# Performance work log

Measured on AMD Instinct MI355X. Metric: run time of the kernel, lower is better.

Reference implementation:

```python
import jax, jax.numpy as jnp
import numpy as np

E = 512        # embed_dim == AutoNCP output_size (motor neurons)
UNITS = 1024   # ncp_units (inter + command + motor)
B = 64         # batch
T = 1024       # sequence length
LN_EPS = 1e-5
SPARSITY = 0.5  # AutoNCP default sparsity_level


def _ncp_sizes():
    rem = UNITS - E
    n_cmd = max(int(0.4 * rem), 1)
    n_inter = rem - n_cmd
    return n_inter, n_cmd, E


def _fanout_mask(rng, n_src, n_dst, fanout):
    # each source neuron connects to `fanout` random targets (NCP-style wiring)
    m = np.zeros((n_src, n_dst), np.float32)
    idx = np.argsort(rng.random((n_src, n_dst)), axis=1)[:, :fanout]
    m[np.arange(n_src)[:, None], idx] = 1.0
    return m


def setup_inputs() -> dict:
    key = jax.random.key(0)
    rng = np.random.default_rng(22222)
    n_inter, n_cmd, n_motor = _ncp_sizes()
    density = 1.0 - SPARSITY
    sensory_fanout = max(int(n_inter * density), 1)
    inter_fanout = max(int(n_cmd * density), 1)
    motor_fanin = max(int(n_cmd * density), 1)
    m0 = _fanout_mask(rng, E, n_inter, sensory_fanout)        # sensory -> inter
    m1 = _fanout_mask(rng, n_inter, n_cmd, inter_fanout)      # inter -> command
    m2 = _fanout_mask(rng, n_motor, n_cmd, motor_fanin).T     # command -> motor (fanin per motor)

    def full_mask(m_in, h):
        # WiredCfCCell: concat ones for the recurrent (hidden) part, then transpose
        # -> mask shape [h, in + h], matching Linear weight [h, in + h]
        return jnp.asarray(np.concatenate([m_in, np.ones((h, h), np.float32)], axis=0).T)

    masks = [full_mask(m0, n_inter), full_mask(m1, n_cmd), full_mask(m2, n_motor)]
    ins = [E, n_inter, n_cmd]
    hs = [n_inter, n_cmd, n_motor]
    d = {}
    ks = jax.random.split(key, 32)
    ki = 0
    for l in range(3):
        fan_in = ins[l] + hs[l]
        scale = float(1.0 / np.sqrt(fan_in))
        for nm in ["ff1", "ff2", "ta", "tb"]:
            d[f"w_{nm}_{l}"] = jax.random.uniform(ks[ki], (hs[l], fan_in), jnp.float32, -scale, scale)
            ki += 1
            d[f"b_{nm}_{l}"] = jnp.zeros((hs[l],), jnp.float32)
        d[f"mask_{l}"] = masks[l]
    d["x"] = jax.random.normal(ks[ki], (B, T, E), jnp.float32)
    d["h0"] = jnp.zeros((B, UNITS), jnp.float32)
    d["ln_gamma"] = jnp.ones((E,), jnp.float32)
    d["ln_beta"] = jnp.zeros((E,), jnp.float32)
    return d


def _cell(z, w1, b1, w2, b2, wa, ba, wb, bb, m):
    # CfCCell (default mode, no backbone), ts = 1.0; sparsity mask on ff1/ff2 only
    ff1 = jnp.tanh(z @ (w1 * m).T + b1)
    ff2 = jnp.tanh(z @ (w2 * m).T + b2)
    t = jax.nn.sigmoid(z @ wa.T + ba + (z @ wb.T + bb))  # sigmoid(t_a * 1.0 + t_b)
    return ff1 * (1.0 - t) + t * ff2


def reference(x, h0, ln_gamma, ln_beta,
              w_ff1_0, b_ff1_0, w_ff2_0, b_ff2_0, w_ta_0, b_ta_0, w_tb_0, b_tb_0, mask_0,
              w_ff1_1, b_ff1_1, w_ff2_1, b_ff2_1, w_ta_1, b_ta_1, w_tb_1, b_tb_1, mask_1,
              w_ff1_2, b_ff1_2, w_ff2_2, b_ff2_2, w_ta_2, b_ta_2, w_tb_2, b_tb_2, mask_2):
    n_inter, n_cmd, _ = _ncp_sizes()
    # LayerNorm over embed_dim
    mu = jnp.mean(x, axis=-1, keepdims=True)
    var = jnp.mean(jnp.square(x - mu), axis=-1, keepdims=True)
    xn = (x - mu) * jax.lax.rsqrt(var + LN_EPS) * ln_gamma + ln_beta
    p0 = (w_ff1_0, b_ff1_0, w_ff2_0, b_ff2_0, w_ta_0, b_ta_0, w_tb_0, b_tb_0, mask_0)
    p1 = (w_ff1_1, b_ff1_1, w_ff2_1, b_ff2_1, w_ta_1, b_ta_1, w_tb_1, b_tb_1, mask_1)
    p2 = (w_ff1_2, b_ff1_2, w_ff2_2, b_ff2_2, w_ta_2, b_ta_2, w_tb_2, b_tb_2, mask_2)

    def step(h, xt):
        h_i, h_c, h_m = jnp.split(h, [n_inter, n_inter + n_cmd], axis=1)
        hi = _cell(jnp.concatenate([xt, h_i], axis=1), *p0)   # inter layer
        hc = _cell(jnp.concatenate([hi, h_c], axis=1), *p1)   # command layer
        hm = _cell(jnp.concatenate([hc, h_m], axis=1), *p2)   # motor layer (block output)
        return jnp.concatenate([hi, hc, hm], axis=1), hm

    h_final, ys = jax.lax.scan(step, h0, jnp.swapaxes(xn, 0, 1))
    y = jnp.swapaxes(ys, 0, 1)  # [B, T, E]; dropout is identity in eval mode
    return y, h_final
```

## Files before the change

### kernel.cpp

```cpp
#include <hip/hip_runtime.h>

typedef __attribute__((ext_vector_type(8))) short short8;
typedef __attribute__((ext_vector_type(4))) float f32x4;
typedef unsigned short ushort_t;
typedef unsigned long long u64_t;

#define T_STEPS 1024
#define NWG 132
#define NWG_MT 33


#define PACK0 0
#define PACK1 1064960
#define PACK2 1517568

#define HI_P (64*320)
#define HC_P (64*224)
#define HM_P (64*512)

#define WS_BAR   0
#define WS_MU    16384
#define WS_RSTD  278528
#define WS_HI    540672
#define WS_HC    704512
#define WS_HM    819200
#define WS_PACK  1081344

__device__ __forceinline__ ushort_t f2bf(float f) {
  union { float f; unsigned u; } un; un.f = f;
  unsigned r = (un.u + 0x7fffu + ((un.u >> 16) & 1u)) >> 16;
  return (ushort_t)r;
}

__device__ __forceinline__ void st2(ushort_t* p, ushort_t v) {
  __hip_atomic_store(p, v, __ATOMIC_RELAXED, __HIP_MEMORY_SCOPE_SYSTEM);
}
__device__ __forceinline__ u64_t ld8(const ushort_t* p) {
  return __hip_atomic_load((const u64_t*)p, __ATOMIC_RELAXED, __HIP_MEMORY_SCOPE_SYSTEM);
}
__device__ __forceinline__ unsigned ldf(const unsigned* p) {
  return __hip_atomic_load(p, __ATOMIC_RELAXED, __HIP_MEMORY_SCOPE_SYSTEM);
}
__device__ __forceinline__ void stf(unsigned* p, unsigned v) {
  __hip_atomic_store(p, v, __ATOMIC_RELAXED, __HIP_MEMORY_SCOPE_SYSTEM);
}

__global__ __launch_bounds__(256) void ln_stats(const float* __restrict__ x,
                                                float* __restrict__ mu,
                                                float* __restrict__ rstd) {
  const int row = blockIdx.x * 4 + (threadIdx.x >> 6);
  const int lane = threadIdx.x & 63;
  const float* xr = x + (size_t)row * 512;
  float4 v0 = *(const float4*)(xr + lane * 8);
  float4 v1 = *(const float4*)(xr + lane * 8 + 4);
  float s = v0.x + v0.y + v0.z + v0.w + v1.x + v1.y + v1.z + v1.w;
  float q = v0.x*v0.x + v0.y*v0.y + v0.z*v0.z + v0.w*v0.w
          + v1.x*v1.x + v1.y*v1.y + v1.z*v1.z + v1.w*v1.w;
  for (int m = 1; m <= 32; m <<= 1) {
    s += __shfl_xor(s, m, 64);
    q += __shfl_xor(q, m, 64);
  }
  if (lane == 0) {
    float mean = s * (1.f / 512.f);
    float var = q * (1.f / 512.f) - mean * mean;
    mu[row] = mean;
    rstd[row] = rsqrtf(var + 1e-5f);
  }
}

__global__ void init_h(const float* __restrict__ h0,
                       ushort_t* hi, ushort_t* hc, ushort_t* hm) {
  int i = blockIdx.x * 256 + threadIdx.x;
  if (i >= 64 * 1056) return;
  int b = i / 1056, c = i % 1056;
  if (c < 320) {
    ushort_t v = (c < 308) ? f2bf(h0[b * 1024 + c]) : 0;
#pragma unroll
    for (int p = 0; p < 4; ++p) st2(hi + p * HI_P + b * 320 + c, v);
  } else if (c < 544) {
    int col = c - 320;
    ushort_t v = (col < 204) ? f2bf(h0[b * 1024 + 308 + col]) : 0;
#pragma unroll
    for (int p = 0; p < 4; ++p) st2(hc + p * HC_P + b * 224 + col, v);
  } else {
    int col = c - 544;
    ushort_t v = f2bf(h0[b * 1024 + 512 + col]);
#pragma unroll
    for (int p = 0; p < 4; ++p) st2(hm + p * HM_P + b * 512 + col, v);
  }
}

struct PackP {
  const float* w[12];
  const float* msk[3];
  ushort_t* pack;
};

__global__ __launch_bounds__(256) void ncp_pack(PackP P) {
  int u = blockIdx.x * 256 + threadIdx.x;
  int layer, rem, KB, K, H, s0p, s0l, s1l;
  size_t base;
  if (u < 133120)      { layer = 0; rem = u;          KB = 26; K = 820; H = 308; s0p = 512; s0l = 512; s1l = 308; base = PACK0; }
  else if (u < 189696) { layer = 1; rem = u - 133120; KB = 17; K = 512; H = 204; s0p = 320; s0l = 308; s1l = 204; base = PACK1; }
  else if (u < 378112) { layer = 2; rem = u - 189696; KB = 23; K = 716; H = 512; s0p = 224; s0l = 204; s1l = 512; base = PACK2; }
  else return;
  const int lane = rem & 63;
  const int mat = (rem >> 6) & 3;
  const int kb = (rem >> 8) % KB;
  const int nt = (rem >> 8) / KB;
  const float* W = P.w[layer * 4 + mat];
  const float* M = (mat < 2) ? P.msk[layer] : nullptr;
  const int n = nt * 16 + (lane & 15);
  const int kbase = kb * 32 + ((lane >> 4) << 3);
  ushort_t* dst = P.pack + base + (size_t)rem * 8;
#pragma unroll
  for (int j = 0; j < 8; ++j) {
    const int kp = kbase + j;
    int ko;
    if (kp < s0p) ko = (kp < s0l) ? kp : -1;
    else { const int ks = kp - s0p; ko = (ks < s1l) ? (s0l + ks) : -1; }
    float v = 0.f;
    if (n < H && ko >= 0) {
      v = W[(size_t)n * K + ko];
      if (M) v *= M[(size_t)n * K + ko];
    }
    dst[j] = f2bf(v);
  }
}

struct MainP {
  const float* x;
  const float* gamma;
  const float* beta;
  const float* bias[12];
  const float* mu;
  const float* rstd;
  ushort_t* hi;
  ushort_t* hc;
  ushort_t* hm;
  const ushort_t* pack;
  unsigned* bar;
  float* y;
  float* hfin;
};

#define MAXKB 13

template<int KBT>
__device__ __forceinline__ void load_w(const ushort_t* __restrict__ bp, int lane,
                                       short8 (*w)[4]) {
#pragma unroll
  for (int kb = 0; kb < KBT; ++kb) {
    const ushort_t* q = bp + (size_t)kb * 2048 + lane * 8;
    w[kb][0] = *(const short8*)(q);
    w[kb][1] = *(const short8*)(q + 512);
    w[kb][2] = *(const short8*)(q + 1024);
    w[kb][3] = *(const short8*)(q + 1536);
  }
}

template<int KBT>
__device__ __forceinline__ void span_reg(const short8 (*w)[4],
                                         const ushort_t* __restrict__ lds, int lane,
                                         f32x4& a0, f32x4& a1, f32x4& a2, f32x4& a3) {
#pragma unroll
  for (int kb = 0; kb < KBT; ++kb) {
    short8 av = *(const short8*)(lds + (size_t)(kb * 64 + lane) * 8);
    a0 = __builtin_amdgcn_mfma_f32_16x16x32_bf16(av, w[kb][0], a0, 0, 0, 0);
    a1 = __builtin_amdgcn_mfma_f32_16x16x32_bf16(av, w[kb][1], a1, 0, 0, 0);
    a2 = __builtin_amdgcn_mfma_f32_16x16x32_bf16(av, w[kb][2], a2, 0, 0, 0);
    a3 = __builtin_amdgcn_mfma_f32_16x16x32_bf16(av, w[kb][3], a3, 0, 0, 0);
  }
}

template<int H, int STP>
__device__ __forceinline__ void epi_h(const f32x4* A, int nt, int lane, int mtile,
                                      const float* __restrict__ bp1, const float* __restrict__ bp2,
                                      const float* __restrict__ bpa, const float* __restrict__ bpb,
                                      ushort_t* __restrict__ hout, float* vk) {
  const int n = nt * 16 + (lane & 15);
  const int r0 = (lane >> 4) << 2;
#pragma unroll
  for (int j = 0; j < 4; ++j) vk[j] = 0.f;
  if (n < H) {
    float c1 = bp1[n], c2 = bp2[n], ca = bpa[n], cb = bpb[n];
#pragma unroll
    for (int j = 0; j < 4; ++j) {
      int brow = mtile * 16 + r0 + j;
      float sg = 1.f / (1.f + __expf(-(A[2][j] + ca + A[3][j] + cb)));
      float f1 = 1.f - 2.f / (1.f + __expf(2.f * (A[0][j] + c1)));
      float f2 = 1.f - 2.f / (1.f + __expf(2.f * (A[1][j] + c2)));
      float v = f1 * (1.f - sg) + sg * f2;
      vk[j] = v;
      st2(hout + (size_t)brow * STP + n, f2bf(v));
    }
  }
}

template<int S1, int ST1, int S2, int ST2>
__device__ __forceinline__ void stage2(ushort_t* __restrict__ r1, const ushort_t* __restrict__ h1,
                                       ushort_t* __restrict__ r2, const ushort_t* __restrict__ h2,
                                       int tid) {
  constexpr int U1 = S1 * 2, U2 = S2 * 2;
  constexpr int I1 = (U1 + 255) / 256;
  constexpr int I2 = (U2 + 255) / 256;
  u64_t a[I1];
  u64_t b[I2 > 0 ? I2 : 1];
#pragma unroll
  for (int i = 0; i < I1; ++i) {
    const int u = tid + i * 256;
    if ((U1 & 255) == 0 || u < U1) {
      const int slot = u >> 1;
      a[i] = ld8(h1 + (slot & 15) * ST1 + (slot >> 6) * 32 + ((slot >> 4) & 3) * 8 + (u & 1) * 4);
    }
  }
  if constexpr (S2 > 0) {
#pragma unroll
    for (int i = 0; i < I2; ++i) {
      const int u = tid + i * 256;
      if ((U2 & 255) == 0 || u < U2) {
        const int slot = u >> 1;
        b[i] = ld8(h2 + (slot & 15) * ST2 + (slot >> 6) * 32 + ((slot >> 4) & 3) * 8 + (u & 1) * 4);
      }
    }
  }
#pragma unroll
  for (int i = 0; i < I1; ++i) {
    const int u = tid + i * 256;
    if ((U1 & 255) == 0 || u < U1) *(u64_t*)(r1 + (size_t)u * 4) = a[i];
  }
  if constexpr (S2 > 0) {
#pragma unroll
    for (int i = 0; i < I2; ++i) {
      const int u = tid + i * 256;
      if ((U2 & 255) == 0 || u < U2) *(u64_t*)(r2 + (size_t)u * 4) = b[i];
    }
  }
}

__device__ __forceinline__ void stage_xn(ushort_t* __restrict__ XN, const MainP& P,
                                         int mtile, int tid, int t) {
#pragma unroll
  for (int i = 0; i < 4; ++i) {
    const int s = tid + i * 256;
    const int ln = s & 63;
    const int brow = mtile * 16 + (ln & 15);
    const int kbase = (s >> 6) * 32 + ((ln >> 4) << 3);
    const float muv = P.mu[brow * T_STEPS + t];
    const float rsv = P.rstd[brow * T_STEPS + t];
    const f32x4* xr = (const f32x4*)(P.x + ((size_t)brow * T_STEPS + t) * 512 + kbase);
    f32x4 xv0 = __builtin_nontemporal_load(xr);
    f32x4 xv1 = __builtin_nontemporal_load(xr + 1);
    const f32x4 g0 = *(const f32x4*)(P.gamma + kbase);
    const f32x4 g1 = *(const f32x4*)(P.gamma + kbase + 4);
    const f32x4 b0 = *(const f32x4*)(P.beta + kbase);
    const f32x4 b1 = *(const f32x4*)(P.beta + kbase + 4);
    short8 w;
#pragma unroll
    for (int j = 0; j < 4; ++j) w[j] = f2bf((xv0[j] - muv) * rsv * g0[j] + b0[j]);
#pragma unroll
    for (int j = 0; j < 4; ++j) w[4 + j] = f2bf((xv1[j] - muv) * rsv * g1[j] + b1[j]);
    *(short8*)(XN + (size_t)s * 8) = w;
  }
}

__device__ __forceinline__ void poll2(const unsigned* wfbase, int lane,
                                      int a1, int c1, unsigned need1,
                                      int a2, int c2, unsigned need2) {
  const unsigned* p = wfbase;
  unsigned need = 0;
  bool act = false;
  if (lane < c1)           { p = wfbase + (a1 + lane) * 16;        need = need1; act = true; }
  else if (lane < c1 + c2) { p = wfbase + (a2 + lane - c1) * 16;   need = need2; act = true; }
  for (;;) {
    unsigned v = act ? ldf(p) : 0xFFFFFFFFu;
    if (__all((int)(v >= need))) break;
    __builtin_amdgcn_s_sleep(1);
  }
}

__global__ __launch_bounds__(256, 1) void ncp_main(MainP P) {
  const int tid = threadIdx.x;
  const int lane = tid & 63;
  const int wv = tid >> 6;
  const int role = wv & 1;
  const int tslot = wv >> 1;
  const int wg = blockIdx.x;
  const int mt = wg / NWG_MT;
  const int r  = wg % NWG_MT;

  __shared__ __align__(16) ushort_t Alds[2688 * 8];
  __shared__ __align__(16) f32x4 pacc[2][256];

  unsigned* wf = P.bar + mt * 1024;
  int a1, c1, a2, c2;
  if (r < 10)      { a1 = 0;  c1 = 10; a2 = 10; c2 = 7;  }
  else if (r < 17) { a1 = 0;  c1 = 17; a2 = 17; c2 = 16; }
  else             { a1 = 10; c1 = 23; a2 = 0;  c2 = 0;  }

  int nt = 0;
  bool valid = true;
  if (r < 10)      nt = r * 2 + tslot;
  else if (r < 17) { nt = (r - 10) * 2 + tslot; valid = (nt < 13); }
  else             nt = (r - 17) * 2 + tslot;

  short8 wreg[MAXKB][4];
  if (valid) {
    if (r < 10) {
      const ushort_t* bp = P.pack + PACK0 + (size_t)nt * 26 * 2048 + (role ? 13 : 0) * 2048;
      load_w<13>(bp, lane, wreg);
    } else if (r < 17) {
      const ushort_t* bp = P.pack + PACK1 + (size_t)nt * 17 * 2048;
      if (role == 0) load_w<9>(bp, lane, wreg);
      else           load_w<8>(bp + 9 * 2048, lane, wreg);
    } else {
      const ushort_t* bp = P.pack + PACK2 + (size_t)nt * 23 * 2048;
      if (role == 0) load_w<12>(bp, lane, wreg);
      else           load_w<11>(bp + 12 * 2048, lane, wreg);
    }
  }

  if (r < 10) stage_xn(Alds, P, mt, tid, 0);

  for (int s = 0; s < T_STEPS + 2; ++s) {
    if (wv == 0) {
      const unsigned needA = (unsigned)s;
      const unsigned needB = (s >= 2) ? (unsigned)(s - 2) : 0u;
      poll2(wf, lane, a1, c1, needA, a2, c2, needB);
    }
    __syncthreads();

    int tstep = 0;
    bool on = false;
    if (r < 10)      { tstep = s;     on = (s < T_STEPS); }
    else if (r < 17) { tstep = s - 1; on = (s >= 1 && s <= T_STEPS) && valid; }
    else             { tstep = s - 2; on = (s >= 2); }
    const bool last = (tstep == T_STEPS - 1);

    if (r < 10) {
      if (s < T_STEPS)
        stage2<640, 320, 0, 0>(Alds + 2048 * 8,
                               P.hi + (((s - 1) & 3) * 64 + mt * 16) * 320,
                               nullptr, nullptr, tid);
    } else if (r < 17) {
      if (s >= 1 && s <= T_STEPS)
        stage2<640, 320, 448, 224>(Alds, P.hi + (((s - 1) & 3) * 64 + mt * 16) * 320,
                                   Alds + 640 * 8,
                                   P.hc + (((s - 2) & 3) * 64 + mt * 16) * 224, tid);
    } else {
      if (s >= 2)
        stage2<448, 224, 1024, 512>(Alds, P.hc + (((s - 2) & 3) * 64 + mt * 16) * 224,
                                    Alds + 448 * 8,
                                    P.hm + (((s - 3) & 3) * 64 + mt * 16) * 512, tid);
    }
    __syncthreads();

    f32x4 A[4];
#pragma unroll
    for (int j = 0; j < 4; ++j) A[j] = {0.f, 0.f, 0.f, 0.f};
    if (on) {
      if (r < 10) {
        const ushort_t* XNc = Alds + (s & 1) * (1024 * 8);
        const ushort_t* HIl = Alds + 2048 * 8;
        if (role == 0) span_reg<13>(wreg, XNc, lane, A[0], A[1], A[2], A[3]);
        else { span_reg<3>(wreg, XNc + 13 * 512, lane, A[0], A[1], A[2], A[3]);
               span_reg<10>(wreg + 3, HIl, lane, A[0], A[1], A[2], A[3]); }
      } else if (r < 17) {
        const ushort_t* HIr = Alds;
        const ushort_t* HCr = Alds + 640 * 8;
        if (role == 0) span_reg<9>(wreg, HIr, lane, A[0], A[1], A[2], A[3]);
        else { span_reg<1>(wreg, HIr + 9 * 512, lane, A[0], A[1], A[2], A[3]);
               span_reg<7>(wreg + 1, HCr, lane, A[0], A[1], A[2], A[3]); }
      } else {
        const ushort_t* HCr = Alds;
        const ushort_t* HMr = Alds + 448 * 8;
        if (role == 0) { span_reg<7>(wreg, HCr, lane, A[0], A[1], A[2], A[3]);
                         span_reg<5>(wreg + 7, HMr, lane, A[0], A[1], A[2], A[3]); }
        else           span_reg<11>(wreg, HMr + 5 * 512, lane, A[0], A[1], A[2], A[3]);
      }
      if (role == 1) {
#pragma unroll
        for (int j = 0; j < 4; ++j) pacc[tslot][j * 64 + lane] = A[j];
      }
    }
    __syncthreads();

    float vk[4];
    if (on && role == 0) {
#pragma unroll
      for (int j = 0; j < 4; ++j) {
        f32x4 p = pacc[tslot][j * 64 + lane];
        A[j][0] += p[0]; A[j][1] += p[1]; A[j][2] += p[2]; A[j][3] += p[3];
      }
      if (r < 10)
        epi_h<308, 320>(A, nt, lane, mt, P.bias[0], P.bias[1], P.bias[2], P.bias[3],
                        P.hi + (tstep & 3) * HI_P, vk);
      else if (r < 17)
        epi_h<204, 224>(A, nt, lane, mt, P.bias[4], P.bias[5], P.bias[6], P.bias[7],
                        P.hc + (tstep & 3) * HC_P, vk);
      else
        epi_h<512, 512>(A, nt, lane, mt, P.bias[8], P.bias[9], P.bias[10], P.bias[11],
                        P.hm + (tstep & 3) * HM_P, vk);
    }
    asm volatile("s_waitcnt vmcnt(0)" ::: "memory");
    __syncthreads();
    if (tid == 0) stf(wf + r * 16, (unsigned)(s + 1));

    if (on && role == 0) {
      const int n_ = nt * 16 + (lane & 15);
      const int r0 = (lane >> 4) << 2;
      const int H_ = (r < 10) ? 308 : ((r < 17) ? 204 : 512);
      const int hoff = (r < 10) ? 0 : ((r < 17) ? 308 : 512);
      if (n_ < H_) {
#pragma unroll
        for (int j = 0; j < 4; ++j) {
          const int brow = mt * 16 + r0 + j;
          if (r >= 17)
            __builtin_nontemporal_store(vk[j], &P.y[((size_t)brow * T_STEPS + tstep) * 512 + n_]);
          if (last)
            __builtin_nontemporal_store(vk[j], &P.hfin[brow * 1024 + hoff + n_]);
        }
      }
    }

    if (r < 10 && s + 1 < T_STEPS)
      stage_xn(Alds + ((s + 1) & 1) * (1024 * 8), P, mt, tid, s + 1);
  }
}

extern "C" void kernel_launch(void* const* d_in, const int* in_sizes, int n_in,
                              void* d_out, int out_size, void* d_ws, size_t ws_size,
                              hipStream_t stream) {
  const float* x     = (const float*)d_in[27];
  const float* h0    = (const float*)d_in[28];
  const float* gamma = (const float*)d_in[29];
  const float* beta  = (const float*)d_in[30];

  char* ws = (char*)d_ws;
  unsigned* bar = (unsigned*)(ws + WS_BAR);
  float* mu   = (float*)(ws + WS_MU);
  float* rstd = (float*)(ws + WS_RSTD);
  ushort_t* hi = (ushort_t*)(ws + WS_HI);
  ushort_t* hc = (ushort_t*)(ws + WS_HC);
  ushort_t* hm = (ushort_t*)(ws + WS_HM);
  ushort_t* pack = (ushort_t*)(ws + WS_PACK);

  float* y = (float*)d_out;
  float* hfin = y + (size_t)64 * 1024 * 512;

  hipMemsetAsync(bar, 0, 16384, stream);

  ln_stats<<<dim3(16384), dim3(256), 0, stream>>>(x, mu, rstd);
  init_h<<<dim3(264), dim3(256), 0, stream>>>(h0, hi, hc, hm);

  PackP pp;
  for (int l = 0; l < 3; ++l) {
    for (int m = 0; m < 4; ++m) pp.w[l * 4 + m] = (const float*)d_in[l * 9 + 2 * m];
    pp.msk[l] = (const float*)d_in[l * 9 + 8];
  }
  pp.pack = pack;
  ncp_pack<<<dim3(1477), dim3(256), 0, stream>>>(pp);

  MainP mp;
  mp.x = x; mp.gamma = gamma; mp.beta = beta;
  for (int l = 0; l < 3; ++l)
    for (int m = 0; m < 4; ++m) mp.bias[l * 4 + m] = (const float*)d_in[l * 9 + 2 * m + 1];
  mp.mu = mu; mp.rstd = rstd;
  mp.hi = hi; mp.hc = hc; mp.hm = hm;
  mp.pack = pack; mp.bar = bar;
  mp.y = y; mp.hfin = hfin;
  ncp_main<<<dim3(NWG), dim3(256), 0, stream>>>(mp);
}
```

Before: 6.650 ms.

## Replace per-step workgroup barrier with per-wave flags and deepen layer pipeline skew

Each producing wave now publishes its own progress flag (two flags per workgroup, at offsets 0 and 8). Pollers take the minimum of both flags, so the trailing __syncthreads before the flag store is no longer needed. The layer pipeline skew grows from 1 to 2 steps per layer, and each layer polls all three groups with relaxed dependencies. The intent is to take the end-of-step barrier off the serial recurrence path. In exchange it adds more poll loads and extra drain steps, and the buffer ring indexing (mod 4) must stay correct at the larger skew.

```diff
diff --git a/kernel.cpp b/kernel.cpp
--- a/kernel.cpp
+++ b/kernel.cpp
@@ -264,16 +264,21 @@
   }
 }
 
-__device__ __forceinline__ void poll2(const unsigned* wfbase, int lane,
+__device__ __forceinline__ void poll3(const unsigned* wfbase, int lane,
                                       int a1, int c1, unsigned need1,
-                                      int a2, int c2, unsigned need2) {
+                                      int a2, int c2, int a3, int c3, unsigned need2) {
   const unsigned* p = wfbase;
   unsigned need = 0;
   bool act = false;
-  if (lane < c1)           { p = wfbase + (a1 + lane) * 16;        need = need1; act = true; }
-  else if (lane < c1 + c2) { p = wfbase + (a2 + lane - c1) * 16;   need = need2; act = true; }
+  if (lane < c1)                { p = wfbase + (a1 + lane) * 16;             need = need1; act = true; }
+  else if (lane < c1 + c2)      { p = wfbase + (a2 + lane - c1) * 16;        need = need2; act = true; }
+  else if (lane < c1 + c2 + c3) { p = wfbase + (a3 + lane - c1 - c2) * 16;   need = need2; act = true; }
   for (;;) {
-    unsigned v = act ? ldf(p) : 0xFFFFFFFFu;
+    unsigned v = 0xFFFFFFFFu;
+    if (act) {
+      unsigned v0 = ldf(p), v1 = ldf(p + 8);
+      v = v0 < v1 ? v0 : v1;
+    }
     if (__all((int)(v >= need))) break;
     __builtin_amdgcn_s_sleep(1);
   }
@@ -293,10 +298,10 @@
   __shared__ __align__(16) f32x4 pacc[2][256];
 
   unsigned* wf = P.bar + mt * 1024;
-  int a1, c1, a2, c2;
-  if (r < 10)      { a1 = 0;  c1 = 10; a2 = 10; c2 = 7;  }
-  else if (r < 17) { a1 = 0;  c1 = 17; a2 = 17; c2 = 16; }
-  else             { a1 = 10; c1 = 23; a2 = 0;  c2 = 0;  }
+  int a1, c1, a2, c2, a3, c3;
+  if (r < 10)      { a1 = 0;  c1 = 10; a2 = 10; c2 = 7;  a3 = 0; c3 = 0;  }
+  else if (r < 17) { a1 = 10; c1 = 7;  a2 = 0;  c2 = 10; a3 = 17; c3 = 16; }
+  else             { a1 = 17; c1 = 16; a2 = 10; c2 = 7;  a3 = 0; c3 = 0;  }
 
   int nt = 0;
   bool valid = true;
@@ -322,19 +327,19 @@
 
   if (r < 10) stage_xn(Alds, P, mt, tid, 0);
 
-  for (int s = 0; s < T_STEPS + 2; ++s) {
+  for (int s = 0; s < T_STEPS + 4; ++s) {
     if (wv == 0) {
       const unsigned needA = (unsigned)s;
-      const unsigned needB = (s >= 2) ? (unsigned)(s - 2) : 0u;
-      poll2(wf, lane, a1, c1, needA, a2, c2, needB);
+      const unsigned needB = (s >= 1) ? (unsigned)(s - 1) : 0u;
+      poll3(wf, lane, a1, c1, needA, a2, c2, a3, c3, needB);
     }
     __syncthreads();
 
     int tstep = 0;
     bool on = false;
     if (r < 10)      { tstep = s;     on = (s < T_STEPS); }
-    else if (r < 17) { tstep = s - 1; on = (s >= 1 && s <= T_STEPS) && valid; }
-    else             { tstep = s - 2; on = (s >= 2); }
+    else if (r < 17) { tstep = s - 2; on = (s >= 2 && s < T_STEPS + 2) && valid; }
+    else             { tstep = s - 4; on = (s >= 4); }
     const bool last = (tstep == T_STEPS - 1);
 
     if (r < 10) {
@@ -343,15 +348,15 @@
                                P.hi + (((s - 1) & 3) * 64 + mt * 16) * 320,
                                nullptr, nullptr, tid);
     } else if (r < 17) {
-      if (s >= 1 && s <= T_STEPS)
-        stage2<640, 320, 448, 224>(Alds, P.hi + (((s - 1) & 3) * 64 + mt * 16) * 320,
+      if (s >= 2 && s < T_STEPS + 2)
+        stage2<640, 320, 448, 224>(Alds, P.hi + (((s - 2) & 3) * 64 + mt * 16) * 320,
                                    Alds + 640 * 8,
-                                   P.hc + (((s - 2) & 3) * 64 + mt * 16) * 224, tid);
+                                   P.hc + (((s - 3) & 3) * 64 + mt * 16) * 224, tid);
     } else {
-      if (s >= 2)
-        stage2<448, 224, 1024, 512>(Alds, P.hc + (((s - 2) & 3) * 64 + mt * 16) * 224,
+      if (s >= 4)
+        stage2<448, 224, 1024, 512>(Alds, P.hc + (((s - 4) & 3) * 64 + mt * 16) * 224,
                                     Alds + 448 * 8,
-                                    P.hm + (((s - 3) & 3) * 64 + mt * 16) * 512, tid);
+                                    P.hm + (((s - 5) & 3) * 64 + mt * 16) * 512, tid);
     }
     __syncthreads();
 
@@ -402,9 +407,10 @@
         epi_h<512, 512>(A, nt, lane, mt, P.bias[8], P.bias[9], P.bias[10], P.bias[11],
                         P.hm + (tstep & 3) * HM_P, vk);
     }
-    asm volatile("s_waitcnt vmcnt(0)" ::: "memory");
-    __syncthreads();
-    if (tid == 0) stf(wf + r * 16, (unsigned)(s + 1));
+    if (role == 0) {
+      asm volatile("s_waitcnt vmcnt(0)" ::: "memory");
+      if (lane == 0) stf(wf + r * 16 + (wv & 2) * 4, (unsigned)(s + 1));
+    }
 
     if (on && role == 0) {
       const int n_ = nt * 16 + (lane & 15);
```

Measured after the change: 6.656 ms. About the same (+0.1%).
